# Kernel tuning notes

Measured on AMD Instinct MI355X. Metric: run time of the kernel, lower is better.

Reference implementation:

```python
import jax, jax.numpy as jnp
import numpy as np

N = 65536
DIMS = [512, 1000, 500, 250, 1]


def setup_inputs() -> dict:
    key = jax.random.key(0)
    ks = jax.random.split(key, 7)

    def init_w(k, fan_in, fan_out):
        return (jax.random.normal(k, (fan_in, fan_out), jnp.float32)
                / np.float32(np.sqrt(fan_in)))

    return {
        "repr_xy_hat": jax.random.normal(ks[0], (N, DIMS[0]), jnp.float32),
        "repr_xy": jax.random.normal(ks[1], (N, DIMS[0]), jnp.float32),
        "W1": init_w(ks[2], DIMS[0], DIMS[1]), "b1": jnp.zeros((DIMS[1],), jnp.float32),
        "W2": init_w(ks[3], DIMS[1], DIMS[2]), "b2": jnp.zeros((DIMS[2],), jnp.float32),
        "W3": init_w(ks[4], DIMS[2], DIMS[3]), "b3": jnp.zeros((DIMS[3],), jnp.float32),
        "W4": init_w(ks[5], DIMS[3], DIMS[4]), "b4": jnp.zeros((DIMS[4],), jnp.float32),
    }


def _disc_logits(x, W1, b1, W2, b2, W3, b3, W4, b4):
    # Batched version of the per-sample Linear-ReLU chain; sigmoid is folded
    # into the numerically stable BCE losses below.
    h = jax.nn.relu(x @ W1 + b1)
    h = jax.nn.relu(h @ W2 + b2)
    h = jax.nn.relu(h @ W3 + b3)
    return (h @ W4 + b4)[:, 0]  # [N]


def reference(repr_xy_hat, repr_xy, W1, b1, W2, b2, W3, b3, W4, b4):
    z_fake = _disc_logits(repr_xy_hat, W1, b1, W2, b2, W3, b3, W4, b4)  # [N]
    z_real = _disc_logits(repr_xy, W1, b1, W2, b2, W3, b3, W4, b4)      # [N]
    # generator loss: sum_i -log sigmoid(z_fake_i) = softplus(-z_fake)
    loss_F = jnp.sum(jax.nn.softplus(-z_fake))
    # discriminator loss: sum_i [-log sigmoid(z_real_i) - log(1 - sigmoid(z_fake_i))]
    # pred is detached in the original -> stop_gradient on the fake logits.
    z_fake_d = jax.lax.stop_gradient(z_fake)
    loss_D = jnp.sum(jax.nn.softplus(-z_real) + jax.nn.softplus(z_fake_d))
    return (loss_F, loss_D)
```

## Files before the change

kernel.cpp:

```cpp
#include <hip/hip_runtime.h>
#include <hip/hip_bf16.h>
#include <cmath>

using short4v = __attribute__((ext_vector_type(4))) short;
using f32x16  = __attribute__((ext_vector_type(16))) float;
using int8v   = __attribute__((ext_vector_type(8))) int;

#define MFMASC(a,b,c) __builtin_amdgcn_mfma_scale_f32_32x32x64_f8f6f4( \
    a, b, c, 0, 0, 0, 0x7F7F7F7F, 0, 0x7F7F7F7F)

__device__ __forceinline__ unsigned short f2bf(float f) {
    union { float f; unsigned u; } v; v.f = f;
    unsigned u = v.u;
    return (unsigned short)((u + 0x7FFFu + ((u >> 16) & 1u)) >> 16);
}
__device__ __forceinline__ float bf2f(unsigned short h) {
    union { unsigned u; float f; } v; v.u = ((unsigned)h) << 16;
    return v.f;
}
__device__ __forceinline__ float softplus(float x) {
    return fmaxf(x, 0.f) + log1pf(expf(-fabsf(x)));
}
__device__ __forceinline__ unsigned f4_to_fp8x4(float a, float b, float c, float d) {
    int v = __builtin_amdgcn_cvt_pk_fp8_f32(a, b, 0, false);
    v = __builtin_amdgcn_cvt_pk_fp8_f32(c, d, v, true);
    return (unsigned)v;
}
__device__ __forceinline__ int8v mk8(uint4 a, uint4 b) {
    int8v r;
    r[0] = (int)a.x; r[1] = (int)a.y; r[2] = (int)a.z; r[3] = (int)a.w;
    r[4] = (int)b.x; r[5] = (int)b.y; r[6] = (int)b.z; r[7] = (int)b.w;
    return r;
}

__global__ void pack_w_fp8g(const float* __restrict__ W, uint4* __restrict__ out,
                            int K_real, int M_real, int KG, int CT) {
    int tid = blockIdx.x * blockDim.x + threadIdx.x;
    if (tid >= CT * KG * 64) return;
    int lane = tid & 63;
    int t    = tid >> 6;
    int kg   = t % KG;
    int ct   = t / KG;
    int m  = ct * 32 + (lane & 31);
    int kb = kg * 64 + ((lane >> 5) << 5);
    float f[32];
#pragma unroll
    for (int j = 0; j < 32; ++j) {
        int k = kb + j;
        f[j] = (k < K_real && m < M_real) ? W[(size_t)k * M_real + m] : 0.f;
    }
    uint4 o0, o1;
    o0.x = f4_to_fp8x4(f[0],  f[1],  f[2],  f[3]);
    o0.y = f4_to_fp8x4(f[4],  f[5],  f[6],  f[7]);
    o0.z = f4_to_fp8x4(f[8],  f[9],  f[10], f[11]);
    o0.w = f4_to_fp8x4(f[12], f[13], f[14], f[15]);
    o1.x = f4_to_fp8x4(f[16], f[17], f[18], f[19]);
    o1.y = f4_to_fp8x4(f[20], f[21], f[22], f[23]);
    o1.z = f4_to_fp8x4(f[24], f[25], f[26], f[27]);
    o1.w = f4_to_fp8x4(f[28], f[29], f[30], f[31]);
    out[(size_t)tid * 2]     = o0;
    out[(size_t)tid * 2 + 1] = o1;
}

__global__ void pack_bias(const float* __restrict__ b1, const float* __restrict__ b2,
                          const float* __restrict__ b3, float* __restrict__ out) {
    int i = blockIdx.x * 256 + threadIdx.x;
    if (i < 1024)      out[i] = (i < 1000) ? b1[i] : 0.f;
    else if (i < 1536) { int j = i - 1024; out[i] = (j < 500) ? b2[j] : 0.f; }
    else if (i < 1792) { int j = i - 1536; out[i] = (j < 250) ? b3[j] : 0.f; }
}

__global__ __launch_bounds__(512, 4) void fused_mlp(
    const float* __restrict__ Xf, const float* __restrict__ Xr,
    const uint4* __restrict__ pW1, const uint4* __restrict__ pW2,
    const uint4* __restrict__ pW3, const float* __restrict__ biasp,
    const float* __restrict__ W4, const float* __restrict__ b4,
    float* __restrict__ partials)
{
    __shared__ __align__(16) unsigned char smem[73728];
    float* red = (float*)smem;

    const int tidx = threadIdx.x;
    const int wid  = tidx >> 6;
    const int lane = tidx & 63;
    const int l31  = lane & 31;
    const int hi   = lane >> 5;
    const int swzx = (l31 & 7) << 4;
    const int swz  = (l31 & 15) << 4;

    const long grow0 = (long)blockIdx.x * 64;
    const float* X = (grow0 < 65536) ? (Xf + (size_t)grow0 * 512)
                                     : (Xr + (size_t)(grow0 - 65536) * 512);

#pragma unroll 1
    for (int p = 0; p < 2; ++p) {
        const uint4* wpA = pW1 + ((size_t)((p * 16 + wid * 2 + 0) * 8) * 64 + lane) * 2;
        const uint4* wpB = pW1 + ((size_t)((p * 16 + wid * 2 + 1) * 8) * 64 + lane) * 2;
        f32x16 acc[2][2];
#pragma unroll
        for (int c = 0; c < 2; ++c)
#pragma unroll
            for (int rt = 0; rt < 2; ++rt)
#pragma unroll
                for (int g = 0; g < 16; ++g) acc[c][rt][g] = 0.f;

#pragma unroll 1
        for (int ch = 0; ch < 4; ++ch) {
            float4 xr[4];
#pragma unroll
            for (int it = 0; it < 4; ++it) {
                int idx = it * 512 + tidx; int r = idx >> 5; int q = idx & 31;
                xr[it] = *(const float4*)(X + (size_t)r * 512 + ch * 128 + q * 4);
            }
            __syncthreads();
#pragma unroll
            for (int it = 0; it < 4; ++it) {
                int idx = it * 512 + tidx; int r = idx >> 5; int k0 = (idx & 31) * 4;
                *(unsigned*)(smem + r * 128 + (k0 ^ ((r & 7) << 4))) =
                    f4_to_fp8x4(xr[it].x, xr[it].y, xr[it].z, xr[it].w);
            }
            __syncthreads();
#pragma unroll
            for (int kgl = 0; kgl < 2; ++kgl) {
                int kg = ch * 2 + kgl;
                int k0 = kgl * 64 + hi * 32;
                const unsigned char* r0 = smem + l31 * 128;
                const unsigned char* r1 = smem + (32 + l31) * 128;
                int8v a0 = mk8(*(const uint4*)(r0 + (k0 ^ swzx)),
                               *(const uint4*)(r0 + ((k0 + 16) ^ swzx)));
                int8v a1 = mk8(*(const uint4*)(r1 + (k0 ^ swzx)),
                               *(const uint4*)(r1 + ((k0 + 16) ^ swzx)));
                int8v w0 = mk8(wpA[(size_t)kg * 128], wpA[(size_t)kg * 128 + 1]);
                int8v w1 = mk8(wpB[(size_t)kg * 128], wpB[(size_t)kg * 128 + 1]);
                acc[0][0] = MFMASC(w0, a0, acc[0][0]);
                acc[0][1] = MFMASC(w0, a1, acc[0][1]);
                acc[1][0] = MFMASC(w1, a0, acc[1][0]);
                acc[1][1] = MFMASC(w1, a1, acc[1][1]);
            }
        }
#pragma unroll
        for (int c = 0; c < 2; ++c) {
            int mt = (p * 16 + wid * 2 + c) * 32;
#pragma unroll
            for (int rt = 0; rt < 2; ++rt) {
                int row = rt * 32 + l31;
#pragma unroll
                for (int q = 0; q < 4; ++q) {
                    int mg = mt + q * 8 + hi * 4;
                    float4 bb = *(const float4*)(biasp + mg);
                    float v0 = fmaxf(acc[c][rt][q * 4 + 0] + bb.x, 0.f);
                    float v1 = fmaxf(acc[c][rt][q * 4 + 1] + bb.y, 0.f);
                    float v2 = fmaxf(acc[c][rt][q * 4 + 2] + bb.z, 0.f);
                    float v3 = fmaxf(acc[c][rt][q * 4 + 3] + bb.w, 0.f);
                    *(unsigned*)(smem + 8192 + row * 1024 + (mg ^ swz)) =
                        f4_to_fp8x4(v0, v1, v2, v3);
                }
            }
        }
    }
    __syncthreads();

    {
        const uint4* wpA = pW2 + ((size_t)((wid * 2 + 0) * 16) * 64 + lane) * 2;
        const uint4* wpB = pW2 + ((size_t)((wid * 2 + 1) * 16) * 64 + lane) * 2;
        f32x16 acc[2][2];
#pragma unroll
        for (int c = 0; c < 2; ++c)
#pragma unroll
            for (int rt = 0; rt < 2; ++rt)
#pragma unroll
                for (int g = 0; g < 16; ++g) acc[c][rt][g] = 0.f;
#pragma unroll 1
        for (int kg = 0; kg < 16; ++kg) {
            int k0 = kg * 64 + hi * 32;
            const unsigned char* r0 = smem + 8192 + l31 * 1024;
            const unsigned char* r1 = smem + 8192 + (32 + l31) * 1024;
            int8v a0 = mk8(*(const uint4*)(r0 + (k0 ^ swz)),
                           *(const uint4*)(r0 + ((k0 + 16) ^ swz)));
            int8v a1 = mk8(*(const uint4*)(r1 + (k0 ^ swz)),
                           *(const uint4*)(r1 + ((k0 + 16) ^ swz)));
            int8v w0 = mk8(wpA[(size_t)kg * 128], wpA[(size_t)kg * 128 + 1]);
            int8v w1 = mk8(wpB[(size_t)kg * 128], wpB[(size_t)kg * 128 + 1]);
            acc[0][0] = MFMASC(w0, a0, acc[0][0]);
            acc[0][1] = MFMASC(w0, a1, acc[0][1]);
            acc[1][0] = MFMASC(w1, a0, acc[1][0]);
            acc[1][1] = MFMASC(w1, a1, acc[1][1]);
        }
        __syncthreads();
#pragma unroll
        for (int c = 0; c < 2; ++c) {
            int mt = (wid * 2 + c) * 32;
#pragma unroll
            for (int rt = 0; rt < 2; ++rt) {
                int row = rt * 32 + l31;
#pragma unroll
                for (int q = 0; q < 4; ++q) {
                    int mg = mt + q * 8 + hi * 4;
                    float4 bb = *(const float4*)(biasp + 1024 + mg);
                    float v0 = fmaxf(acc[c][rt][q * 4 + 0] + bb.x, 0.f);
                    float v1 = fmaxf(acc[c][rt][q * 4 + 1] + bb.y, 0.f);
                    float v2 = fmaxf(acc[c][rt][q * 4 + 2] + bb.z, 0.f);
                    float v3 = fmaxf(acc[c][rt][q * 4 + 3] + bb.w, 0.f);
                    *(unsigned*)(smem + 8192 + row * 512 + (mg ^ swz)) =
                        f4_to_fp8x4(v0, v1, v2, v3);
                }
            }
        }
    }
    __syncthreads();

    {
        const uint4* wp = pW3 + ((size_t)(wid * 8) * 64 + lane) * 2;
        f32x16 acc3[2];
#pragma unroll
        for (int rt = 0; rt < 2; ++rt)
#pragma unroll
            for (int g = 0; g < 16; ++g) acc3[rt][g] = 0.f;
#pragma unroll 1
        for (int kg = 0; kg < 8; ++kg) {
            int k0 = kg * 64 + hi * 32;
            const unsigned char* r0 = smem + 8192 + l31 * 512;
            const unsigned char* r1 = smem + 8192 + (32 + l31) * 512;
            int8v a0 = mk8(*(const uint4*)(r0 + (k0 ^ swz)),
                           *(const uint4*)(r0 + ((k0 + 16) ^ swz)));
            int8v a1 = mk8(*(const uint4*)(r1 + (k0 ^ swz)),
                           *(const uint4*)(r1 + ((k0 + 16) ^ swz)));
            int8v w = mk8(wp[(size_t)kg * 128], wp[(size_t)kg * 128 + 1]);
            acc3[0] = MFMASC(w, a0, acc3[0]);
            acc3[1] = MFMASC(w, a1, acc3[1]);
        }
        int mt = wid * 32;
#pragma unroll
        for (int rt = 0; rt < 2; ++rt) {
            int row = rt * 32 + l31;
#pragma unroll
            for (int q = 0; q < 4; ++q) {
                int mg = mt + q * 8 + hi * 4;
                float4 bb = *(const float4*)(biasp + 1536 + mg);
                short4v s;
                s[0] = (short)f2bf(fmaxf(acc3[rt][q * 4 + 0] + bb.x, 0.f));
                s[1] = (short)f2bf(fmaxf(acc3[rt][q * 4 + 1] + bb.y, 0.f));
                s[2] = (short)f2bf(fmaxf(acc3[rt][q * 4 + 2] + bb.z, 0.f));
                s[3] = (short)f2bf(fmaxf(acc3[rt][q * 4 + 3] + bb.w, 0.f));
                *(short4v*)(smem + 40960 + row * 512 + ((mg * 2) ^ swz)) = s;
            }
        }
    }
    __syncthreads();

    {
        int g  = tidx >> 3;
        int t8 = tidx & 7;
        int gs = (g & 15) << 4;
        float sum = 0.f;
#pragma unroll
        for (int o = 0; o < 4; ++o) {
            int colb = t8 * 32 + o * 8;
            short4v v0 = *(const short4v*)(smem + 40960 + g * 512 + ((colb * 2) ^ gs));
            short4v v1 = *(const short4v*)(smem + 40960 + g * 512 + ((colb * 2 + 8) ^ gs));
#pragma unroll
            for (int j = 0; j < 4; ++j) {
                int c0 = colb + j, c1 = colb + 4 + j;
                if (c0 < 250) sum += bf2f((unsigned short)v0[j]) * W4[c0];
                if (c1 < 250) sum += bf2f((unsigned short)v1[j]) * W4[c1];
            }
        }
        sum += __shfl_down(sum, 4, 8);
        sum += __shfl_down(sum, 2, 8);
        sum += __shfl_down(sum, 1, 8);
        if (t8 == 0) {
            float z = sum + b4[0];
            bool fake = (grow0 < 65536);
            float spn = softplus(-z);
            red[g]      = fake ? spn : 0.f;
            red[64 + g] = fake ? softplus(z) : spn;
        }
    }
    __syncthreads();
    if (tidx == 0) {
        float pF = 0.f, pD = 0.f;
        for (int i = 0; i < 64; ++i) { pF += red[i]; pD += red[64 + i]; }
        partials[(size_t)blockIdx.x * 2]     = pF;
        partials[(size_t)blockIdx.x * 2 + 1] = pD;
    }
}

__global__ void reduce_partials(const float* __restrict__ partials, int nblocks,
                                float* __restrict__ out) {
    __shared__ float sF[256], sD[256];
    float f = 0.f, d = 0.f;
    for (int i = threadIdx.x; i < nblocks; i += 256) {
        f += partials[2 * i];
        d += partials[2 * i + 1];
    }
    sF[threadIdx.x] = f; sD[threadIdx.x] = d;
    __syncthreads();
    for (int s = 128; s > 0; s >>= 1) {
        if (threadIdx.x < s) {
            sF[threadIdx.x] += sF[threadIdx.x + s];
            sD[threadIdx.x] += sD[threadIdx.x + s];
        }
        __syncthreads();
    }
    if (threadIdx.x == 0) { out[0] = sF[0]; out[1] = sD[0]; }
}

extern "C" void kernel_launch(void* const* d_in, const int* in_sizes, int n_in,
                              void* d_out, int out_size, void* d_ws, size_t ws_size,
                              hipStream_t stream) {
    const float* Xf = (const float*)d_in[0];
    const float* Xr = (const float*)d_in[1];
    const float* W1 = (const float*)d_in[2];
    const float* b1 = (const float*)d_in[3];
    const float* W2 = (const float*)d_in[4];
    const float* b2 = (const float*)d_in[5];
    const float* W3 = (const float*)d_in[6];
    const float* b3 = (const float*)d_in[7];
    const float* W4 = (const float*)d_in[8];
    const float* b4 = (const float*)d_in[9];

    uint4* pW1 = (uint4*)d_ws;
    uint4* pW2 = pW1 + 32768;
    uint4* pW3 = pW2 + 32768;
    float* biasp = (float*)(pW3 + 8192);
    float* partials = biasp + 2048;

    pack_w_fp8g<<<(32 * 8 * 64) / 256, 256, 0, stream>>>(W1, pW1, 512, 1000, 8, 32);
    pack_w_fp8g<<<(16 * 16 * 64) / 256, 256, 0, stream>>>(W2, pW2, 1000, 500, 16, 16);
    pack_w_fp8g<<<(8 * 8 * 64) / 256, 256, 0, stream>>>(W3, pW3, 500, 250, 8, 8);
    pack_bias<<<7, 256, 0, stream>>>(b1, b2, b3, biasp);

    fused_mlp<<<2048, 512, 0, stream>>>(Xf, Xr, pW1, pW2, pW3,
                                        biasp, W4, b4, partials);

    reduce_partials<<<1, 256, 0, stream>>>(partials, 2048, (float*)d_out);
}
```

Before: 213.2 us.

## Stage full fp8 input tile in LDS once and reuse across layer-1 passes

Loads the entire 64x512 input tile into shared memory as fp8 once, instead of reloading and reconverting it in chunks for each of the two layer-1 output passes. The layer-1 activations are written in place over the staged input, with an extra barrier before pass 2 overwrites the input half. This halves global reads of the large input and removes many per-chunk barriers, but the load is no longer interleaved with MFMA work. Shared memory shrinks, and the later layer buffers are re-offset.

```diff
diff --git a/kernel.cpp b/kernel.cpp
--- a/kernel.cpp
+++ b/kernel.cpp
@@ -77,20 +77,39 @@
     const float* __restrict__ W4, const float* __restrict__ b4,
     float* __restrict__ partials)
 {
-    __shared__ __align__(16) unsigned char smem[73728];
-    float* red = (float*)smem;
+    __shared__ __align__(16) unsigned char smem[66048];
+    float* red = (float*)(smem + 65536);
 
     const int tidx = threadIdx.x;
     const int wid  = tidx >> 6;
     const int lane = tidx & 63;
     const int l31  = lane & 31;
     const int hi   = lane >> 5;
-    const int swzx = (l31 & 7) << 4;
     const int swz  = (l31 & 15) << 4;
 
     const long grow0 = (long)blockIdx.x * 64;
     const float* X = (grow0 < 65536) ? (Xf + (size_t)grow0 * 512)
                                      : (Xr + (size_t)(grow0 - 65536) * 512);
+
+#pragma unroll 1
+    for (int gb = 0; gb < 4; ++gb) {
+        float4 xr[4];
+#pragma unroll
+        for (int it = 0; it < 4; ++it) {
+            int idx = (gb * 4 + it) * 512 + tidx;
+            int r = idx >> 7; int k0 = (idx & 127) * 4;
+            xr[it] = *(const float4*)(X + (size_t)r * 512 + k0);
+        }
+#pragma unroll
+        for (int it = 0; it < 4; ++it) {
+            int idx = (gb * 4 + it) * 512 + tidx;
+            int r = idx >> 7; int k0 = (idx & 127) * 4;
+            int pos = 512 + ((k0 & 0x1F0) ^ ((r & 15) << 4)) + (k0 & 12);
+            *(unsigned*)(smem + r * 1024 + pos) =
+                f4_to_fp8x4(xr[it].x, xr[it].y, xr[it].z, xr[it].w);
+        }
+    }
+    __syncthreads();
 
 #pragma unroll 1
     for (int p = 0; p < 2; ++p) {
@@ -105,76 +124,10 @@
                 for (int g = 0; g < 16; ++g) acc[c][rt][g] = 0.f;
 
 #pragma unroll 1
-        for (int ch = 0; ch < 4; ++ch) {
-            float4 xr[4];
-#pragma unroll
-            for (int it = 0; it < 4; ++it) {
-                int idx = it * 512 + tidx; int r = idx >> 5; int q = idx & 31;
-                xr[it] = *(const float4*)(X + (size_t)r * 512 + ch * 128 + q * 4);
-            }
-            __syncthreads();
-#pragma unroll
-            for (int it = 0; it < 4; ++it) {
-                int idx = it * 512 + tidx; int r = idx >> 5; int k0 = (idx & 31) * 4;
-                *(unsigned*)(smem + r * 128 + (k0 ^ ((r & 7) << 4))) =
-                    f4_to_fp8x4(xr[it].x, xr[it].y, xr[it].z, xr[it].w);
-            }
-            __syncthreads();
-#pragma unroll
-            for (int kgl = 0; kgl < 2; ++kgl) {
-                int kg = ch * 2 + kgl;
-                int k0 = kgl * 64 + hi * 32;
-                const unsigned char* r0 = smem + l31 * 128;
-                const unsigned char* r1 = smem + (32 + l31) * 128;
-                int8v a0 = mk8(*(const uint4*)(r0 + (k0 ^ swzx)),
-                               *(const uint4*)(r0 + ((k0 + 16) ^ swzx)));
-                int8v a1 = mk8(*(const uint4*)(r1 + (k0 ^ swzx)),
-                               *(const uint4*)(r1 + ((k0 + 16) ^ swzx)));
-                int8v w0 = mk8(wpA[(size_t)kg * 128], wpA[(size_t)kg * 128 + 1]);
-                int8v w1 = mk8(wpB[(size_t)kg * 128], wpB[(size_t)kg * 128 + 1]);
-                acc[0][0] = MFMASC(w0, a0, acc[0][0]);
-                acc[0][1] = MFMASC(w0, a1, acc[0][1]);
-                acc[1][0] = MFMASC(w1, a0, acc[1][0]);
-                acc[1][1] = MFMASC(w1, a1, acc[1][1]);
-            }
-        }
-#pragma unroll
-        for (int c = 0; c < 2; ++c) {
-            int mt = (p * 16 + wid * 2 + c) * 32;
-#pragma unroll
-            for (int rt = 0; rt < 2; ++rt) {
-                int row = rt * 32 + l31;
-#pragma unroll
-                for (int q = 0; q < 4; ++q) {
-                    int mg = mt + q * 8 + hi * 4;
-                    float4 bb = *(const float4*)(biasp + mg);
-                    float v0 = fmaxf(acc[c][rt][q * 4 + 0] + bb.x, 0.f);
-                    float v1 = fmaxf(acc[c][rt][q * 4 + 1] + bb.y, 0.f);
-                    float v2 = fmaxf(acc[c][rt][q * 4 + 2] + bb.z, 0.f);
-                    float v3 = fmaxf(acc[c][rt][q * 4 + 3] + bb.w, 0.f);
-                    *(unsigned*)(smem + 8192 + row * 1024 + (mg ^ swz)) =
-                        f4_to_fp8x4(v0, v1, v2, v3);
-                }
-            }
-        }
-    }
-    __syncthreads();
-
-    {
-        const uint4* wpA = pW2 + ((size_t)((wid * 2 + 0) * 16) * 64 + lane) * 2;
-        const uint4* wpB = pW2 + ((size_t)((wid * 2 + 1) * 16) * 64 + lane) * 2;
-        f32x16 acc[2][2];
-#pragma unroll
-        for (int c = 0; c < 2; ++c)
-#pragma unroll
-            for (int rt = 0; rt < 2; ++rt)
-#pragma unroll
-                for (int g = 0; g < 16; ++g) acc[c][rt][g] = 0.f;
-#pragma unroll 1
-        for (int kg = 0; kg < 16; ++kg) {
+        for (int kg = 0; kg < 8; ++kg) {
             int k0 = kg * 64 + hi * 32;
-            const unsigned char* r0 = smem + 8192 + l31 * 1024;
-            const unsigned char* r1 = smem + 8192 + (32 + l31) * 1024;
+            const unsigned char* r0 = smem + l31 * 1024 + 512;
+            const unsigned char* r1 = smem + (32 + l31) * 1024 + 512;
             int8v a0 = mk8(*(const uint4*)(r0 + (k0 ^ swz)),
                            *(const uint4*)(r0 + ((k0 + 16) ^ swz)));
             int8v a1 = mk8(*(const uint4*)(r1 + (k0 ^ swz)),
@@ -186,6 +139,55 @@
             acc[1][0] = MFMASC(w1, a0, acc[1][0]);
             acc[1][1] = MFMASC(w1, a1, acc[1][1]);
         }
+        if (p == 1) __syncthreads();
+#pragma unroll
+        for (int c = 0; c < 2; ++c) {
+            int mt = (p * 16 + wid * 2 + c) * 32;
+#pragma unroll
+            for (int rt = 0; rt < 2; ++rt) {
+                int row = rt * 32 + l31;
+#pragma unroll
+                for (int q = 0; q < 4; ++q) {
+                    int mg = mt + q * 8 + hi * 4;
+                    float4 bb = *(const float4*)(biasp + mg);
+                    float v0 = fmaxf(acc[c][rt][q * 4 + 0] + bb.x, 0.f);
+                    float v1 = fmaxf(acc[c][rt][q * 4 + 1] + bb.y, 0.f);
+                    float v2 = fmaxf(acc[c][rt][q * 4 + 2] + bb.z, 0.f);
+                    float v3 = fmaxf(acc[c][rt][q * 4 + 3] + bb.w, 0.f);
+                    *(unsigned*)(smem + row * 1024 + (mg ^ swz)) =
+                        f4_to_fp8x4(v0, v1, v2, v3);
+                }
+            }
+        }
+    }
+    __syncthreads();
+
+    {
+        const uint4* wpA = pW2 + ((size_t)((wid * 2 + 0) * 16) * 64 + lane) * 2;
+        const uint4* wpB = pW2 + ((size_t)((wid * 2 + 1) * 16) * 64 + lane) * 2;
+        f32x16 acc[2][2];
+#pragma unroll
+        for (int c = 0; c < 2; ++c)
+#pragma unroll
+            for (int rt = 0; rt < 2; ++rt)
+#pragma unroll
+                for (int g = 0; g < 16; ++g) acc[c][rt][g] = 0.f;
+#pragma unroll 1
+        for (int kg = 0; kg < 16; ++kg) {
+            int k0 = kg * 64 + hi * 32;
+            const unsigned char* r0 = smem + l31 * 1024;
+            const unsigned char* r1 = smem + (32 + l31) * 1024;
+            int8v a0 = mk8(*(const uint4*)(r0 + (k0 ^ swz)),
+                           *(const uint4*)(r0 + ((k0 + 16) ^ swz)));
+            int8v a1 = mk8(*(const uint4*)(r1 + (k0 ^ swz)),
+                           *(const uint4*)(r1 + ((k0 + 16) ^ swz)));
+            int8v w0 = mk8(wpA[(size_t)kg * 128], wpA[(size_t)kg * 128 + 1]);
+            int8v w1 = mk8(wpB[(size_t)kg * 128], wpB[(size_t)kg * 128 + 1]);
+            acc[0][0] = MFMASC(w0, a0, acc[0][0]);
+            acc[0][1] = MFMASC(w0, a1, acc[0][1]);
+            acc[1][0] = MFMASC(w1, a0, acc[1][0]);
+            acc[1][1] = MFMASC(w1, a1, acc[1][1]);
+        }
         __syncthreads();
 #pragma unroll
         for (int c = 0; c < 2; ++c) {
@@ -201,7 +203,7 @@
                     float v1 = fmaxf(acc[c][rt][q * 4 + 1] + bb.y, 0.f);
                     float v2 = fmaxf(acc[c][rt][q * 4 + 2] + bb.z, 0.f);
                     float v3 = fmaxf(acc[c][rt][q * 4 + 3] + bb.w, 0.f);
-                    *(unsigned*)(smem + 8192 + row * 512 + (mg ^ swz)) =
+                    *(unsigned*)(smem + row * 512 + (mg ^ swz)) =
                         f4_to_fp8x4(v0, v1, v2, v3);
                 }
             }
@@ -219,8 +221,8 @@
 #pragma unroll 1
         for (int kg = 0; kg < 8; ++kg) {
             int k0 = kg * 64 + hi * 32;
-            const unsigned char* r0 = smem + 8192 + l31 * 512;
-            const unsigned char* r1 = smem + 8192 + (32 + l31) * 512;
+            const unsigned char* r0 = smem + l31 * 512;
+            const unsigned char* r1 = smem + (32 + l31) * 512;
             int8v a0 = mk8(*(const uint4*)(r0 + (k0 ^ swz)),
                            *(const uint4*)(r0 + ((k0 + 16) ^ swz)));
             int8v a1 = mk8(*(const uint4*)(r1 + (k0 ^ swz)),
@@ -242,7 +244,7 @@
                 s[1] = (short)f2bf(fmaxf(acc3[rt][q * 4 + 1] + bb.y, 0.f));
                 s[2] = (short)f2bf(fmaxf(acc3[rt][q * 4 + 2] + bb.z, 0.f));
                 s[3] = (short)f2bf(fmaxf(acc3[rt][q * 4 + 3] + bb.w, 0.f));
-                *(short4v*)(smem + 40960 + row * 512 + ((mg * 2) ^ swz)) = s;
+                *(short4v*)(smem + 32768 + row * 512 + ((mg * 2) ^ swz)) = s;
             }
         }
     }
@@ -256,8 +258,8 @@
 #pragma unroll
         for (int o = 0; o < 4; ++o) {
             int colb = t8 * 32 + o * 8;
-            short4v v0 = *(const short4v*)(smem + 40960 + g * 512 + ((colb * 2) ^ gs));
-            short4v v1 = *(const short4v*)(smem + 40960 + g * 512 + ((colb * 2 + 8) ^ gs));
+            short4v v0 = *(const short4v*)(smem + 32768 + g * 512 + ((colb * 2) ^ gs));
+            short4v v1 = *(const short4v*)(smem + 32768 + g * 512 + ((colb * 2 + 8) ^ gs));
 #pragma unroll
             for (int j = 0; j < 4; ++j) {
                 int c0 = colb + j, c1 = colb + 4 + j;
```

Result: faster. 189.9 us (-10.9%).
